# Kernel tuning notes

Measured on AMD Instinct MI355X. Metric: run time of the kernel, lower is better.

Reference implementation:

```python
import jax, jax.numpy as jnp
import numpy as np

# ---- static config (mirrors PaCoVoxelLoss init) ----
NUM_QUERIES = 20
FACTOR = 64
NUM_GT = 12
K_NEIGHBORS = 8          # repulsion.num_neighbors
REP_EPS = 1e-12          # repulsion.epsilon
BANDWIDTH = 0.03         # repulsion.kernel_bandwidth
RADIUS = 0.07            # repulsion.radius
ALPHA_PARAM = 0.5
BETA_CHAMFER = 20.0
W_CLS, W_REP, W_CH1, W_CH2 = 1.0, 1.0, 1.0, 1.0
PAD_COST = 1e6           # pad value to square the rectangular assignment problem


def _hungarian(cost):
    # Jonker-Volgenant / e-maxx shortest augmenting path; cost: (n, n) float64.
    # Returns col_to_row: for each column j, the row assigned to it.
    n = cost.shape[0]
    INF = 1e18
    u = np.zeros(n + 1); v = np.zeros(n + 1)
    p = np.zeros(n + 1, dtype=np.int64)
    way = np.zeros(n + 1, dtype=np.int64)
    for i in range(1, n + 1):
        p[0] = i; j0 = 0
        minv = np.full(n + 1, INF)
        used = np.zeros(n + 1, dtype=bool)
        while True:
            used[j0] = True
            i0 = p[j0]; delta = INF; j1 = 0
            for j in range(1, n + 1):
                if not used[j]:
                    cur = cost[i0 - 1, j - 1] - u[i0] - v[j]
                    if cur < minv[j]:
                        minv[j] = cur; way[j] = j0
                    if minv[j] < delta:
                        delta = minv[j]; j1 = j
            for j in range(n + 1):
                if used[j]:
                    u[p[j]] += delta; v[j] -= delta
                else:
                    minv[j] -= delta
            j0 = j1
            if p[j0] == 0:
                break
        while j0 != 0:
            j1 = way[j0]; p[j0] = p[j1]; j0 = j1
    return p[1:] - 1


def _match(cost_np):
    # cost_np: (B, Q, P) with P <= Q -> rows (B, P): pred row matched to each gt col.
    Bn, Qn, Pn = cost_np.shape
    rows = np.zeros((Bn, Pn), dtype=np.int64)
    for b in range(Bn):
        sq = np.full((Qn, Qn), PAD_COST, dtype=np.float64)
        sq[:, :Pn] = cost_np[b].astype(np.float64)
        rows[b] = _hungarian(sq)[:Pn]
    return rows


def _gather_q(A, rows):
    # A: (B, Q, P), rows: (B, P) -> A[b, rows[b,p], p] : (B, P)
    return jnp.take_along_axis(A, rows[:, None, :], axis=1)[:, 0, :]


def _bce_logits(x, t):
    return jnp.maximum(x, 0.0) - x * t + jnp.log1p(jnp.exp(-jnp.abs(x)))


def _cost_terms(pred_normals, pred_distances, gt_normals, gt_distances, points, gt_masks):
    mask_f = gt_masks.astype(points.dtype)           # (B, P, N)
    cnt = mask_f.sum(-1)                             # (B, P)
    # |points . n_q - d_q| for all query planes: (B, Q, N)
    pp = jnp.abs(jnp.einsum('bnd,bqd->bqn', points, pred_normals) - pred_distances[:, :, None])
    cham_raw = jnp.einsum('bqn,bpn->bqp', pp, mask_f) / jnp.maximum(cnt, 1.0)[:, None, :]
    has = (cnt > 0)[:, None, :]                      # (B, 1, P)
    normal_sim = 1.0 - jnp.abs(jnp.einsum('bqd,bpd->bqp', pred_normals, gt_normals))
    dist_diff = jnp.abs(pred_distances[:, :, None] - gt_distances[:, None, :])
    cost = normal_sim + 0.5 * dist_diff + 5.0 * jnp.where(has, cham_raw, 1.0)
    return cost, cham_raw, normal_sim, dist_diff, has


def _losses(pred_logits, pred_normals, pred_distances, gt_normals, gt_distances,
            points, reconstructed_points, gt, gt_masks, rows):
    _, cham_raw, normal_sim, dist_diff, has = _cost_terms(
        pred_normals, pred_distances, gt_normals, gt_distances, points, gt_masks)

    # classification loss: target 1 at matched pred rows
    Qn = pred_logits.shape[1]
    cls_target = jax.nn.one_hot(rows, Qn, dtype=pred_logits.dtype).sum(axis=1)  # (B, Q)
    cls_loss = _bce_logits(pred_logits, cls_target).mean()

    # param loss over matched pairs (mean over P matches, mean over B)
    param_loss = (_gather_q(normal_sim, rows).mean(-1) + _gather_q(dist_diff, rows).mean(-1)).mean()

    # pvd chamfer: point-to-plane term, zero for empty masks, /P /B
    pvd_chamfer = _gather_q(jnp.where(has, cham_raw, 0.0), rows).mean()

    # repulsion loss on per-query point groups
    Bn = reconstructed_points.shape[0]
    rp = reconstructed_points.reshape(Bn, NUM_QUERIES, FACTOR, 3)
    d2 = jnp.sum((rp[:, :, :, None, :] - rp[:, :, None, :, :]) ** 2, axis=-1)  # (B,Q,F,F)
    _, idx = jax.lax.top_k(-d2, K_NEIGHBORS)       # k nearest incl. self
    dn = jnp.maximum(jnp.take_along_axis(d2, idx[..., 1:], axis=-1), REP_EPS)  # (B,Q,F,k-1)
    w = jnp.exp(-dn / BANDWIDTH ** 2)
    rep = jnp.maximum(jnp.mean((RADIUS - jnp.sqrt(dn)) * w, axis=(2, 3)), 0.0).mean()

    # fine-grained chamfer (L1 and L2) between reconstructed and gt clouds
    diff = reconstructed_points[:, :, None, :] - gt[:, None, :, :]  # (B, M, G, 3)
    d1 = jnp.abs(diff).sum(-1)
    d2c = (diff ** 2).sum(-1)
    ch1 = (0.5 * (d1.min(axis=2).mean(axis=1) + d1.min(axis=1).mean(axis=1))).mean()
    ch2 = (0.5 * (d2c.min(axis=2).mean(axis=1) + d2c.min(axis=1).mean(axis=1))).mean()

    total = (W_CLS * cls_loss + ALPHA_PARAM * param_loss + BETA_CHAMFER * pvd_chamfer
             + W_REP * rep + W_CH1 * ch1 + W_CH2 * ch2)
    return total


def setup_inputs() -> dict:
    key = jax.random.key(0)
    ks = jax.random.split(key, 10)
    B, Q, P, N, G = 8, NUM_QUERIES, NUM_GT, 4096, 2048

    def unit(k, shape):
        v = jax.random.normal(k, shape, dtype=jnp.float32)
        return v / jnp.linalg.norm(v, axis=-1, keepdims=True)

    return {
        'pred_logits': jax.random.normal(ks[0], (B, Q), dtype=jnp.float32),
        'pred_normals': unit(ks[1], (B, Q, 3)),
        'pred_distances': jax.random.normal(ks[2], (B, Q), dtype=jnp.float32),
        'gt_normals': unit(ks[3], (B, P, 3)),
        'gt_distances': jax.random.normal(ks[4], (B, P), dtype=jnp.float32),
        'gt_masks': jax.random.bernoulli(ks[5], 0.3, (B, P, N)),
        'points': jax.random.normal(ks[6], (B, N, 3), dtype=jnp.float32),
        'reconstructed_points': 0.5 * jax.random.normal(ks[7], (B, Q * FACTOR, 3), dtype=jnp.float32),
        'gt': jax.random.normal(ks[8], (B, G, 3), dtype=jnp.float32),
        'gt_index': jax.random.randint(ks[9], (B, G), 0, P, dtype=jnp.int64) if jax.config.jax_enable_x64 else jax.random.randint(ks[9], (B, G), 0, P, dtype=jnp.int32),
    }


def reference(pred_logits, pred_normals, pred_distances, gt_normals, gt_distances,
              points, reconstructed_points, gt, gt_masks, gt_index):
    cost = _cost_terms(pred_normals, pred_distances, gt_normals, gt_distances, points, gt_masks)[0]
    rows = jnp.asarray(_match(np.asarray(cost)))  # Hungarian (host, like scipy in original)
    return _losses(pred_logits, pred_normals, pred_distances, gt_normals, gt_distances,
                   points, reconstructed_points, gt, gt_masks, rows)
```

## Files before the change

kernel.cpp:

```cpp
#include <hip/hip_runtime.h>
#include <math.h>

#define Bn 8
#define Qn 20
#define Pn 12
#define Nn 4096
#define Gn 2048
#define Mn 1280
#define Fn 64
#define KNB 7
#define SA 8
#define SB 5
#define DONE_TARGET 113


__device__ __forceinline__ float aread(float* p) { return atomicAdd(p, 0.0f); }

__device__ __forceinline__ void contribute(float* acc, int* done, float* out) {
    __threadfence();
    int old = atomicAdd(done, 1);
    if (old == DONE_TARGET - 1) {
        __threadfence();
        float a0 = aread(&acc[0]);
        float a1 = aread(&acc[1]);
        float a2 = aread(&acc[2]);
        float a3 = aread(&acc[3]);
        float a4 = aread(&acc[4]);
        float a5 = aread(&acc[5]);
        out[0] = a0 + 0.5f * a1 + 20.f * a2 + a3 + a4 + a5;
    }
}

__global__ void mega1_kernel(const float* __restrict__ pred_normals,
                             const float* __restrict__ pred_distances,
                             const float* __restrict__ gt_normals,
                             const float* __restrict__ gt_distances,
                             const float* __restrict__ points,
                             const int*   __restrict__ gt_masks,
                             const float* __restrict__ recon,
                             const float* __restrict__ gt,
                             float* __restrict__ ws) {
    __shared__ float smem[2 * Pn * 256];
    const int blk = blockIdx.x;
    const int tid = threadIdx.x;

    float* cham = ws;
    float* ns   = ws + 1920;
    float* dd   = ws + 3840;
    float* cost = ws + 5760;
    float* cnt  = ws + 7680;
    float* acc  = ws + 7776;
    float* rep_part = ws + 7808;
    float* pmA1 = ws + 8192;
    float* pmA2 = ws + 90112;
    float* pmB1 = ws + 172032;
    float* pmB2 = ws + 253952;

    if (blk < 160) {
        if (blk == 0 && tid < 8) acc[tid] = 0.f;
        const int b = blk / Qn, q = blk % Qn;
        const float nx = pred_normals[(b * Qn + q) * 3 + 0];
        const float ny = pred_normals[(b * Qn + q) * 3 + 1];
        const float nz = pred_normals[(b * Qn + q) * 3 + 2];
        const float dq = pred_distances[b * Qn + q];

        float accs[Pn], accw[Pn];
#pragma unroll
        for (int p = 0; p < Pn; ++p) { accs[p] = 0.f; accw[p] = 0.f; }

        const float* ptb = points + (size_t)b * Nn * 3;
        const int*   mb  = gt_masks + (size_t)b * Pn * Nn;

        for (int n = tid; n < Nn; n += 256) {
            float px = ptb[n * 3 + 0], py = ptb[n * 3 + 1], pz = ptb[n * 3 + 2];
            float pp = fabsf(px * nx + py * ny + pz * nz - dq);
#pragma unroll
            for (int p = 0; p < Pn; ++p) {
                float m = (float)mb[(size_t)p * Nn + n];
                accs[p] += pp * m;
                accw[p] += m;
            }
        }
#pragma unroll
        for (int p = 0; p < Pn; ++p) {
            smem[p * 256 + tid] = accs[p];
            smem[(p + Pn) * 256 + tid] = accw[p];
        }
        __syncthreads();
        for (int off = 128; off > 0; off >>= 1) {
            if (tid < off) {
#pragma unroll
                for (int r = 0; r < 2 * Pn; ++r) smem[r * 256 + tid] += smem[r * 256 + tid + off];
            }
            __syncthreads();
        }
        if (tid < Pn) {
            const int p = tid;
            float c  = smem[(p + Pn) * 256];
            float cv = smem[p * 256] / fmaxf(c, 1.f);
            float gnx = gt_normals[(b * Pn + p) * 3 + 0];
            float gny = gt_normals[(b * Pn + p) * 3 + 1];
            float gnz = gt_normals[(b * Pn + p) * 3 + 2];
            float nsim = 1.f - fabsf(nx * gnx + ny * gny + nz * gnz);
            float ddv  = fabsf(dq - gt_distances[b * Pn + p]);
            int idx = (b * Qn + q) * Pn + p;
            cham[idx] = cv;
            ns[idx]   = nsim;
            dd[idx]   = ddv;
            cost[idx] = nsim + 0.5f * ddv + 5.f * ((c > 0.f) ? cv : 1.f);
            if (q == 0) cnt[b * Pn + p] = c;
        }
    } else if (blk < 200) {
        const int wave = tid >> 6, lane = tid & 63;
        const int g = (blk - 160) * 4 + wave;
        float* xs = smem + wave * 192;
        float* ys = xs + 64;
        float* zs = xs + 128;
        const float* base = recon + (size_t)g * Fn * 3;
        xs[lane] = base[lane * 3 + 0];
        ys[lane] = base[lane * 3 + 1];
        zs[lane] = base[lane * 3 + 2];
        float best[KNB];
#pragma unroll
        for (int k = 0; k < KNB; ++k) best[k] = 3.4e38f;
        const float xi = xs[lane], yi = ys[lane], zi = zs[lane];
        for (int j = 0; j < Fn; ++j) {
            if (j == lane) continue;
            float dx = xi - xs[j], dy = yi - ys[j], dz = zi - zs[j];
            float d2 = dx * dx + dy * dy + dz * dz;
            if (d2 < best[KNB - 1]) {
                int k = KNB - 1;
                while (k > 0 && best[k - 1] > d2) { best[k] = best[k - 1]; --k; }
                best[k] = d2;
            }
        }
        float sum = 0.f;
#pragma unroll
        for (int k = 0; k < KNB; ++k) {
            float dn = fmaxf(best[k], 1e-12f);
            float w  = expf(-dn / (0.03f * 0.03f));
            sum += (0.07f - sqrtf(dn)) * w;
        }
        for (int off = 32; off > 0; off >>= 1) sum += __shfl_down(sum, off);
        if (lane == 0) rep_part[g] = fmaxf(sum / (float)(Fn * KNB), 0.f);
    } else {
        int cblk = blk - 200;
        float* tx = smem;
        float* ty = smem + 256;
        float* tz = smem + 512;
        float x, y, z;
        const float* inner;
        float *o1, *o2;
        int idx;
        if (cblk < 40 * SA) {
            int s = cblk % SA, ob = cblk / SA;
            idx = ob * 256 + tid;
            int b = idx / Mn;
            x = recon[idx * 3 + 0]; y = recon[idx * 3 + 1]; z = recon[idx * 3 + 2];
            inner = gt + ((size_t)b * Gn + s * 256) * 3;
            o1 = pmA1 + s * (Bn * Mn); o2 = pmA2 + s * (Bn * Mn);
        } else {
            cblk -= 40 * SA;
            int s = cblk % SB, ob = cblk / SB;
            idx = ob * 256 + tid;
            int b = idx / Gn;
            x = gt[idx * 3 + 0]; y = gt[idx * 3 + 1]; z = gt[idx * 3 + 2];
            inner = recon + ((size_t)b * Mn + s * 256) * 3;
            o1 = pmB1 + s * (Bn * Gn); o2 = pmB2 + s * (Bn * Gn);
        }
        tx[tid] = inner[tid * 3 + 0];
        ty[tid] = inner[tid * 3 + 1];
        tz[tid] = inner[tid * 3 + 2];
        __syncthreads();
        float m1 = 3.4e38f, m2 = 3.4e38f;
        for (int j = 0; j < 256; ++j) {
            float dx = x - tx[j], dy = y - ty[j], dz = z - tz[j];
            float d1 = fabsf(dx) + fabsf(dy) + fabsf(dz);
            float d2 = dx * dx + dy * dy + dz * dz;
            m1 = fminf(m1, d1); m2 = fminf(m2, d2);
        }
        o1[idx] = m1; o2[idx] = m2;
    }
}

__global__ void finale_kernel(const float* __restrict__ pred_logits,
                              float* __restrict__ ws, float* __restrict__ out) {
    const int blk = blockIdx.x;
    const int tid = threadIdx.x;

    float* cham = ws;
    float* ns   = ws + 1920;
    float* dd   = ws + 3840;
    float* cost = ws + 5760;
    float* cnt  = ws + 7680;
    float* acc  = ws + 7776;
    int*   done = (int*)(ws + 7782);
    float* rep_part = ws + 7808;
    float* pmA1 = ws + 8192;
    float* pmA2 = ws + 90112;
    float* pmB1 = ws + 172032;
    float* pmB2 = ws + 253952;

    if (blk < 8) {
        if (tid >= 64) return;
        const int b = blk;
        const int t = tid;
        __shared__ double hsm[Pn * Qn];
        for (int k = t; k < Qn * Pn; k += 64)
            hsm[(k % Pn) * Qn + (k / Pn)] = (double)cost[b * Qn * Pn + k];

        const int col = t;
        const bool isCol = (col >= 1 && col <= Qn);
        double v = 0.0, u = 0.0, minv = 0.0;
        int way = 0, p = 0;

        for (int i = 1; i <= Pn; ++i) {
            const int p0 = i;
            minv = 1e18;
            bool used = false;
            bool rowInPath = false;
            int j0 = 0;
            while (true) {
                if (col == j0) used = true;
                int i0 = (j0 == 0) ? p0 : __shfl(p, j0);
                if (t == i0) rowInPath = true;
                double u_i0 = __shfl(u, i0);
                double mv = 1e18;
                if (isCol && !used) {
                    double cur = hsm[(i0 - 1) * Qn + (col - 1)] - u_i0 - v;
                    if (cur < minv) { minv = cur; way = j0; }
                    mv = minv;
                }
                double bv = mv; int bj = col;
#pragma unroll
                for (int off = 16; off > 0; off >>= 1) {
                    double ov = __shfl_down(bv, off);
                    int    oj = __shfl_down(bj, off);
                    if (ov < bv) { bv = ov; bj = oj; }
                }
                double delta = __shfl(bv, 0);
                int    j1    = __shfl(bj, 0);
                if (used || col == 0) v -= delta;
                else if (isCol)       minv -= delta;
                if (rowInPath)        u += delta;
                j0 = j1;
                int pj0 = __shfl(p, j0);
                if (pj0 == 0) break;
            }
            while (j0 != 0) {
                int wj = __shfl(way, j0);
                int pw = (wj == 0) ? p0 : __shfl(p, wj);
                if (col == j0) p = pw;
                j0 = wj;
            }
        }

        float cls = 0.f, par = 0.f, pvd = 0.f;
        if (isCol) {
            float x = pred_logits[b * Qn + (col - 1)];
            float tgt = (p > 0) ? 1.f : 0.f;
            cls = fmaxf(x, 0.f) - x * tgt + log1pf(expf(-fabsf(x)));
            if (p > 0) {
                int idx = (b * Qn + (col - 1)) * Pn + (p - 1);
                par = ns[idx] + dd[idx];
                pvd = (cnt[b * Pn + (p - 1)] > 0.f) ? cham[idx] : 0.f;
            }
        }
        for (int off = 32; off > 0; off >>= 1) {
            cls += __shfl_down(cls, off);
            par += __shfl_down(par, off);
            pvd += __shfl_down(pvd, off);
        }
        if (t == 0) {
            atomicAdd(&acc[0], cls / (float)(Bn * Qn));
            atomicAdd(&acc[1], par / (float)(Bn * Pn));
            atomicAdd(&acc[2], pvd / (float)(Bn * Pn));
            contribute(acc, done, out);
        }
        return;
    }

    __shared__ float s1[256], s2[256];
    const int cblk = blk - 8;
    float c1 = 0.f, c2 = 0.f;
    if (cblk < 40) {
        int idx = cblk * 256 + tid;
        float m1 = 3.4e38f, m2 = 3.4e38f;
#pragma unroll
        for (int s = 0; s < SA; ++s) {
            m1 = fminf(m1, pmA1[s * (Bn * Mn) + idx]);
            m2 = fminf(m2, pmA2[s * (Bn * Mn) + idx]);
        }
        c1 = m1 * (0.5f / (float)(Bn * Mn));
        c2 = m2 * (0.5f / (float)(Bn * Mn));
    } else if (cblk < 104) {
        int idx = (cblk - 40) * 256 + tid;
        float m1 = 3.4e38f, m2 = 3.4e38f;
#pragma unroll
        for (int s = 0; s < SB; ++s) {
            m1 = fminf(m1, pmB1[s * (Bn * Gn) + idx]);
            m2 = fminf(m2, pmB2[s * (Bn * Gn) + idx]);
        }
        c1 = m1 * (0.5f / (float)(Bn * Gn));
        c2 = m2 * (0.5f / (float)(Bn * Gn));
    } else {
        c1 = (tid < Bn * Qn) ? rep_part[tid] / (float)(Bn * Qn) : 0.f;
    }
    s1[tid] = c1; s2[tid] = c2;
    __syncthreads();
    for (int off = 128; off > 0; off >>= 1) {
        if (tid < off) { s1[tid] += s1[tid + off]; s2[tid] += s2[tid + off]; }
        __syncthreads();
    }
    if (tid == 0) {
        if (cblk < 104) {
            atomicAdd(&acc[4], s1[0]);
            atomicAdd(&acc[5], s2[0]);
        } else {
            atomicAdd(&acc[3], s1[0]);
        }
        contribute(acc, done, out);
    }
}

extern "C" void kernel_launch(void* const* d_in, const int* in_sizes, int n_in,
                              void* d_out, int out_size, void* d_ws, size_t ws_size,
                              hipStream_t stream) {
    const float* pred_logits    = (const float*)d_in[0];
    const float* pred_normals   = (const float*)d_in[1];
    const float* pred_distances = (const float*)d_in[2];
    const float* gt_normals     = (const float*)d_in[3];
    const float* gt_distances   = (const float*)d_in[4];
    const int*   gt_masks       = (const int*)d_in[5];
    const float* points         = (const float*)d_in[6];
    const float* recon          = (const float*)d_in[7];
    const float* gt             = (const float*)d_in[8];

    mega1_kernel<<<840, 256, 0, stream>>>(pred_normals, pred_distances, gt_normals,
                                          gt_distances, points, gt_masks, recon, gt,
                                          (float*)d_ws);
    finale_kernel<<<113, 256, 0, stream>>>(pred_logits, (float*)d_ws, (float*)d_out);
}
```

Measured before the change: 132.5 us.

## Speed up wave-level Hungarian solver and branchless kNN insertion

The Hungarian loop keeps each column's costs in registers instead of shared memory, uses readlane for uniform broadcasts instead of ds_bpermute shuffles, and packs the min value and column index into one sortable 64-bit key for the argmin reduction. The repulsion kNN swaps the data-dependent insertion sort for a branchless min/max insertion network. The aim is to shorten the serial latency chain of the single-wave matching and remove divergence in the kNN loop. The packed key drops the low 6 mantissa bits of delta, which slightly perturbs the exact double values used in matching.

```diff
diff --git a/kernel.cpp b/kernel.cpp
--- a/kernel.cpp
+++ b/kernel.cpp
@@ -29,6 +29,22 @@
         float a5 = aread(&acc[5]);
         out[0] = a0 + 0.5f * a1 + 20.f * a2 + a3 + a4 + a5;
     }
+}
+
+__device__ __forceinline__ int rdlane_i(int v, int l) {
+    return __builtin_amdgcn_readlane(v, l);
+}
+__device__ __forceinline__ double rdlane_d(double v, int l) {
+    int lo = __builtin_amdgcn_readlane(__double2loint(v), l);
+    int hi = __builtin_amdgcn_readlane(__double2hiint(v), l);
+    return __hiloint2double(hi, lo);
+}
+__device__ __forceinline__ unsigned long long shfl_down_u64(unsigned long long x, int off) {
+    unsigned int lo = (unsigned int)(x & 0xFFFFFFFFULL);
+    unsigned int hi = (unsigned int)(x >> 32);
+    lo = __shfl_down(lo, off);
+    hi = __shfl_down(hi, off);
+    return ((unsigned long long)hi << 32) | lo;
 }
 
 __global__ void mega1_kernel(const float* __restrict__ pred_normals,
@@ -125,13 +141,15 @@
         for (int k = 0; k < KNB; ++k) best[k] = 3.4e38f;
         const float xi = xs[lane], yi = ys[lane], zi = zs[lane];
         for (int j = 0; j < Fn; ++j) {
-            if (j == lane) continue;
             float dx = xi - xs[j], dy = yi - ys[j], dz = zi - zs[j];
             float d2 = dx * dx + dy * dy + dz * dz;
-            if (d2 < best[KNB - 1]) {
-                int k = KNB - 1;
-                while (k > 0 && best[k - 1] > d2) { best[k] = best[k - 1]; --k; }
-                best[k] = d2;
+            d2 = (j == lane) ? 3.4e38f : d2;
+#pragma unroll
+            for (int k = 0; k < KNB; ++k) {
+                float lo = fminf(best[k], d2);
+                float hi = fmaxf(best[k], d2);
+                best[k] = lo;
+                d2 = hi;
             }
         }
         float sum = 0.f;
@@ -205,12 +223,18 @@
         if (tid >= 64) return;
         const int b = blk;
         const int t = tid;
-        __shared__ double hsm[Pn * Qn];
-        for (int k = t; k < Qn * Pn; k += 64)
-            hsm[(k % Pn) * Qn + (k / Pn)] = (double)cost[b * Qn * Pn + k];
-
         const int col = t;
         const bool isCol = (col >= 1 && col <= Qn);
+
+        double c[Pn];
+#pragma unroll
+        for (int k = 0; k < Pn; ++k) c[k] = 0.0;
+        if (isCol) {
+            const float* cb = cost + ((size_t)b * Qn + (col - 1)) * Pn;
+#pragma unroll
+            for (int k = 0; k < Pn; ++k) c[k] = (double)cb[k];
+        }
+
         double v = 0.0, u = 0.0, minv = 0.0;
         int way = 0, p = 0;
 
@@ -219,39 +243,50 @@
             minv = 1e18;
             bool used = false;
             bool rowInPath = false;
-            int j0 = 0;
+            int j0s = 0;
             while (true) {
-                if (col == j0) used = true;
-                int i0 = (j0 == 0) ? p0 : __shfl(p, j0);
-                if (t == i0) rowInPath = true;
-                double u_i0 = __shfl(u, i0);
-                double mv = 1e18;
+                if (col == j0s) used = true;
+                int i0s = (j0s == 0) ? p0 : rdlane_i(p, j0s);
+                if (t == i0s) rowInPath = true;
+                double u_i0 = rdlane_d(u, i0s);
+                double cij = c[0];
+#pragma unroll
+                for (int k = 1; k < Pn; ++k) cij = (i0s == k + 1) ? c[k] : cij;
                 if (isCol && !used) {
-                    double cur = hsm[(i0 - 1) * Qn + (col - 1)] - u_i0 - v;
-                    if (cur < minv) { minv = cur; way = j0; }
-                    mv = minv;
+                    double cur = cij - u_i0 - v;
+                    if (cur < minv) { minv = cur; way = j0s; }
                 }
-                double bv = mv; int bj = col;
+                double mv = (isCol && !used) ? minv : 1e18;
+                long long sbits = __double_as_longlong(mv);
+                unsigned long long key = (unsigned long long)sbits;
+                key = (sbits < 0) ? ~key : (key | 0x8000000000000000ULL);
+                key = (key & ~63ULL) | (unsigned long long)(unsigned)col;
 #pragma unroll
                 for (int off = 16; off > 0; off >>= 1) {
-                    double ov = __shfl_down(bv, off);
-                    int    oj = __shfl_down(bj, off);
-                    if (ov < bv) { bv = ov; bj = oj; }
+                    unsigned long long o = shfl_down_u64(key, off);
+                    key = (o < key) ? o : key;
                 }
-                double delta = __shfl(bv, 0);
-                int    j1    = __shfl(bj, 0);
+                int klo = rdlane_i((int)(unsigned)(key & 0xFFFFFFFFULL), 0);
+                int khi = rdlane_i((int)(unsigned)(key >> 32), 0);
+                unsigned long long kmin =
+                    ((unsigned long long)(unsigned)khi << 32) | (unsigned)klo;
+                int j1 = (int)(kmin & 63ULL);
+                unsigned long long ub = kmin & ~63ULL;
+                long long sres = (ub >> 63) ? (long long)(ub ^ 0x8000000000000000ULL)
+                                            : ~(long long)ub;
+                double delta = __longlong_as_double(sres);
                 if (used || col == 0) v -= delta;
                 else if (isCol)       minv -= delta;
                 if (rowInPath)        u += delta;
-                j0 = j1;
-                int pj0 = __shfl(p, j0);
+                j0s = j1;
+                int pj0 = rdlane_i(p, j0s);
                 if (pj0 == 0) break;
             }
-            while (j0 != 0) {
-                int wj = __shfl(way, j0);
-                int pw = (wj == 0) ? p0 : __shfl(p, wj);
-                if (col == j0) p = pw;
-                j0 = wj;
+            while (j0s != 0) {
+                int wj = rdlane_i(way, j0s);
+                int pw = (wj == 0) ? p0 : rdlane_i(p, wj);
+                if (col == j0s) p = pw;
+                j0s = wj;
             }
         }
 
```

Result: faster. 121.1 us (-8.6%).
